# Performance work log

Hardware: AMD Instinct MI355X
Metric: run time of the kernel (lower is better)

## Reference

```python
import jax, jax.numpy as jnp
import numpy as np

NB, NA, NG, T = 16, 3, 64, 60
EPS = 1e-16


def cal_gous(pd, gt):
    # pd: [N,4], gt: [M,4], boxes as (cx, cy, w, h), normalized. Returns IoU, GIoU [N,M].
    px1 = pd[:, 0] - pd[:, 2] / 2; px2 = pd[:, 0] + pd[:, 2] / 2
    py1 = pd[:, 1] - pd[:, 3] / 2; py2 = pd[:, 1] + pd[:, 3] / 2
    gx1 = gt[:, 0] - gt[:, 2] / 2; gx2 = gt[:, 0] + gt[:, 2] / 2
    gy1 = gt[:, 1] - gt[:, 3] / 2; gy2 = gt[:, 1] + gt[:, 3] / 2
    iw = jnp.clip(jnp.minimum(px2[:, None], gx2[None, :]) - jnp.maximum(px1[:, None], gx1[None, :]), 0.0)
    ih = jnp.clip(jnp.minimum(py2[:, None], gy2[None, :]) - jnp.maximum(py1[:, None], gy1[None, :]), 0.0)
    inter = iw * ih
    pa = (pd[:, 2] * pd[:, 3])[:, None]
    ga = (gt[:, 2] * gt[:, 3])[None, :]
    union = pa + ga - inter
    iou = inter / (union + EPS)
    cw = jnp.maximum(px2[:, None], gx2[None, :]) - jnp.minimum(px1[:, None], gx1[None, :])
    ch = jnp.maximum(py2[:, None], gy2[None, :]) - jnp.minimum(py1[:, None], gy1[None, :])
    ca = cw * ch
    gou = iou - (ca - union) / (ca + EPS)
    return iou, gou


def build_target(labels, nB, nA, nG):
    # Vectorized version of my_build_target: occurrence-rank anchor assignment + scatter.
    g = labels[:, 1:] * nG
    gxs, gys, gws, ghs = g[:, 0], g[:, 1], g[:, 2], g[:, 3]
    b = labels[:, 0].astype(jnp.int32)
    gi = gxs.astype(jnp.int32)
    gj = gys.astype(jnp.int32)
    key = (b * nG + gj) * nG + gi  # cell identity incl. batch
    n = labels.shape[0]
    le = jnp.arange(n)[:, None] <= jnp.arange(n)[None, :]
    # occ[j] = number of earlier (or same) targets sharing the cell, minus 1 -> anchor slot
    occ = ((key[:, None] == key[None, :]) & le).sum(axis=0) - 1
    a = jnp.minimum(occ, nA)  # targets with occ >= nA scatter into dummy slot nA (discarded)

    def scat(vals):
        return jnp.zeros((nB, nA + 1, nG, nG), jnp.float32).at[b, a, gj, gi].set(vals)[:, :nA]

    tx = scat(gxs - jnp.floor(gxs))
    ty = scat(gys - jnp.floor(gys))
    tw = scat(gws / nG)
    th = scat(ghs / nG)
    obj = jnp.zeros((nB, nA + 1, nG, nG), bool).at[b, a, gj, gi].set(True)[:, :nA]
    return obj, tx, ty, tw, th


def _forward(out, labels, int_out, heatmaps):
    nb, nc, nG, _ = out.shape
    nA = nc // 5
    N = nA * nG * nG
    Tn = labels.shape[0] // nb  # equal targets per image by construction
    pred = out.reshape(nb, nA, 5, nG, nG).transpose(0, 1, 3, 4, 2)
    s = jax.nn.sigmoid(pred)
    xs, ys, ws, hs, conf = (s[..., i] for i in range(5))
    gx = jnp.arange(nG, dtype=jnp.float32)[None, None, None, :]
    gy = jnp.arange(nG, dtype=jnp.float32)[None, None, :, None]
    pd_bboxes = jnp.stack([(xs + gx) / nG, (ys + gy) / nG, ws, hs], axis=-1)

    obj, tx, ty, tw, th = build_target(labels, nb, nA, nG)
    objf = obj.astype(jnp.float32)
    cnt = objf.sum()
    loss_xy = (((xs - tx) ** 2 + (ys - ty) ** 2) * objf).sum() / cnt
    tw_s = jnp.where(obj, tw, 1.0); th_s = jnp.where(obj, th, 1.0)
    ws_s = jnp.where(obj, ws, 1.0); hs_s = jnp.where(obj, hs, 1.0)
    loss_wh = (((jnp.log(ws_s) - jnp.log(tw_s)) ** 2 + (jnp.log(hs_s) - jnp.log(th_s)) ** 2) * objf).sum() / cnt

    gts_b = labels.reshape(nb, Tn, 5)[:, :, 1:]
    ious, gous = jax.vmap(cal_gous)(pd_bboxes.reshape(nb, N, 4), gts_b)  # [nb,N,T]
    pd_gous = gous.max(axis=2)
    indices = gous.argmax(axis=2)
    pd_ious = jnp.take_along_axis(ious, indices[..., None], axis=2)[..., 0]  # [nb,N]
    mask = pd_ious >= 0.5
    gt_gous = gous.max(axis=1)
    inds = gous.argmax(axis=1)  # [nb,T] best pred per gt
    loss_gou = jnp.mean(1.0 - gt_gous)
    iou_best = jnp.take_along_axis(ious, inds[:, None, :], axis=1)[:, 0, :]
    loss_iou = jnp.mean(1.0 - iou_best)
    mask_ = jax.vmap(lambda i: jnp.zeros((N,), bool).at[i].set(True))(inds)
    mask2 = (mask | mask_).astype(jnp.float32)
    ignore = ((~mask) | mask_).astype(jnp.float32)
    c2 = mask2.sum(axis=1)
    loss_gou = loss_gou + jnp.mean(((1.0 - pd_gous) * mask2).sum(1) / c2)
    loss_iou = loss_iou + jnp.mean(((1.0 - pd_ious) * mask2).sum(1) / c2)

    conf_f = conf.reshape(nb, N)
    tconfb = (obj.reshape(nb, N) | mask_).astype(jnp.float32)
    inter = (conf_f * tconfb * ignore).sum(1)
    pa = (conf_f ** 2 * ignore).sum(1)
    ga = (tconfb * ignore).sum(1)  # tconfb^2 == tconfb
    loss_conf_b = jnp.mean(1.0 - (2.0 * inter + 1.0) / (pa + ga + 1.0))
    ig = (conf * objf).sum(); pg = (conf ** 2).sum(); gg = objf.sum()
    dice_g = (2.0 * ig + 1.0) / (pg + gg + 1.0)
    dice_g = jnp.where(jnp.isnan(dice_g), 1.0, dice_g)
    loss_conf = (1.0 - dice_g) + loss_conf_b

    total = loss_xy + loss_wh + loss_conf + loss_gou
    heatmap_loss = jnp.mean((int_out - heatmaps) ** 2, axis=(1, 2, 3, 4)).sum() / 4.0
    return jnp.stack([loss_xy, loss_wh, loss_conf, loss_iou, loss_gou, total, heatmap_loss])


def setup_inputs() -> dict:
    key = jax.random.key(0)
    k1, k2, k3, k4, k5 = jax.random.split(key, 5)
    out = jax.random.normal(k1, (NB, NA * 5, NG, NG), jnp.float32)
    b = jnp.repeat(jnp.arange(NB), T).astype(jnp.float32)
    xy = jax.random.uniform(k2, (NB * T, 2), jnp.float32, 0.02, 0.98)
    wh = jax.random.uniform(k3, (NB * T, 2), jnp.float32, 0.05, 0.30)
    labels = jnp.concatenate([b[:, None], xy, wh], axis=1)  # [nGts,5]: (batch, cx, cy, w, h)
    int_out = jax.random.uniform(k4, (4, NB, NA, NG, NG), jnp.float32)
    heatmaps = jax.random.uniform(k5, (4, NB, NA, NG, NG), jnp.float32)
    return {"out": out, "labels": labels, "int_out": int_out, "heatmaps": heatmaps}


def reference(out, labels, int_out, heatmaps):
    return _forward(out, labels, int_out, heatmaps)
```

## Files before the change

### kernel.cpp

```cpp
#include <hip/hip_runtime.h>

#define NBATCH 16
#define NANCH  3
#define NGRID  64
#define NT     60
#define NPB    (NANCH*NGRID*NGRID)
#define NCELL  (NBATCH*NPB)
#define NLBL   (NBATCH*NT)
#define NBPB   (NPB/256)
#define NBLKB  (NBATCH*NBPB)
#define FEPS   1e-16f

__device__ __forceinline__ float frcp(float x) { return __builtin_amdgcn_rcpf(x); }
__device__ __forceinline__ float sigm(float x) { return frcp(1.0f + __expf(-x)); }

__device__ __forceinline__ float waveSum(float v) {
#pragma unroll
    for (int o = 32; o > 0; o >>= 1) v += __shfl_down(v, o, 64);
    return v;
}
__device__ __forceinline__ double waveSumD(double v) {
#pragma unroll
    for (int o = 32; o > 0; o >>= 1) v += __shfl_down(v, o, 64);
    return v;
}

__device__ __forceinline__ unsigned int ford(float f) {
    unsigned int u = __float_as_uint(f);
    return (u & 0x80000000u) ? ~u : (u | 0x80000000u);
}
__device__ __forceinline__ float ford_inv(unsigned int u) {
    unsigned int v = (u & 0x80000000u) ? (u & 0x7fffffffu) : ~u;
    return __uint_as_float(v);
}

__device__ __forceinline__ float gou_f(float px1, float py1, float px2, float py2, float pa,
                                       float gx1, float gy1, float gx2, float gy2, float ga) {
    float iw = fmaxf(fminf(px2, gx2) - fmaxf(px1, gx1), 0.f);
    float ih = fmaxf(fminf(py2, gy2) - fmaxf(py1, gy1), 0.f);
    float inter = iw * ih;
    float un = pa + ga - inter;
    float cw = fmaxf(px2, gx2) - fminf(px1, gx1);
    float ch = fmaxf(py2, gy2) - fminf(py1, gy1);
    float ca = cw * ch;
    float ue = un + FEPS, ce = ca + FEPS;
    return (inter * ce - (ca - un) * ue) * frcp(ue * ce);
}
__device__ __forceinline__ float iou_f(float px1, float py1, float px2, float py2, float pa,
                                       float gx1, float gy1, float gx2, float gy2, float ga) {
    float iw = fmaxf(fminf(px2, gx2) - fmaxf(px1, gx1), 0.f);
    float ih = fmaxf(fminf(py2, gy2) - fmaxf(py1, gy1), 0.f);
    float inter = iw * ih;
    float un = pa + ga - inter;
    return inter * frcp(un + FEPS);
}

__global__ __launch_bounds__(256)
void kB(const float* __restrict__ out, const float* __restrict__ labels,
        const float4* __restrict__ io4, const float4* __restrict__ hm4,
        unsigned long long* __restrict__ gtpart, float4* __restrict__ gtaux,
        double* __restrict__ bpart, unsigned int* __restrict__ ticket) {
    int blk = blockIdx.x, thr = threadIdx.x;
    if (blk == 0 && thr == 0) *ticket = 0u;

    int b = blk / NBPB;
    int s = blk - b * NBPB;
    int n = s * 256 + thr;
    int idx = b * NPB + n;
    int wave = thr >> 6, lane = thr & 63;

    __shared__ float4 G4[NT];
    __shared__ float  GA[NT];
    __shared__ float4 Bxy[256];
    __shared__ float  Bpa[256];
    __shared__ float  pdG[256], pdI[256], cfL[256];
    __shared__ unsigned long long W[4][NT];
    __shared__ unsigned int obits[8];
    __shared__ int keys[NT];
    __shared__ float red[8][4];

    if (thr < 8) obits[thr] = 0u;
    if (thr < NT) {
        const float* lp = labels + (b * NT + thr) * 5;
        float gx = lp[1], gy = lp[2], gw = lp[3], gh = lp[4];
        G4[thr] = make_float4(gx - gw * 0.5f, gy - gh * 0.5f,
                              gx + gw * 0.5f, gy + gh * 0.5f);
        GA[thr] = gw * gh;
        keys[thr] = ((int)(gy * (float)NGRID) << 6) | (int)(gx * (float)NGRID);
    }

    int a = n >> 12, gj = (n >> 6) & 63, gi = n & 63;
    int base = ((b * NANCH * 5 + a * 5) * NGRID + gj) * NGRID + gi;
    float xs = sigm(out[base]);
    float ys = sigm(out[base + NGRID * NGRID]);
    float ws = sigm(out[base + 2 * NGRID * NGRID]);
    float hs = sigm(out[base + 3 * NGRID * NGRID]);
    float cf = sigm(out[base + 4 * NGRID * NGRID]);

    float bx = (xs + (float)gi) * (1.0f / NGRID);
    float by = (ys + (float)gj) * (1.0f / NGRID);
    float px1 = bx - ws * 0.5f, px2 = bx + ws * 0.5f;
    float py1 = by - hs * 0.5f, py2 = by + hs * 0.5f;
    float pa = ws * hs;

    Bxy[thr] = make_float4(px1, py1, px2, py2);
    Bpa[thr] = pa;
    cfL[thr] = cf;
    __syncthreads();

    if (thr < NT) {
        int key = keys[thr];
        int occ = 0;
        for (int i = 0; i < thr; ++i)
            if (keys[i] == key) occ++;
        if (occ < NANCH) {
            int cell = (occ << 12) | key;
            int lc = cell - s * 256;
            if (lc >= 0 && lc < 256) atomicOr(&obits[lc >> 5], 1u << (lc & 31));
        }
    }

    float bg = -1e30f;
    int bt = 0;
    for (int t = 0; t < NT; ++t) {
        float4 g = G4[t];
        float gou = gou_f(px1, py1, px2, py2, pa, g.x, g.y, g.z, g.w, GA[t]);
        if (gou > bg) { bg = gou; bt = t; }
    }
    float4 gbt = G4[bt];
    float biou = iou_f(px1, py1, px2, py2, pa, gbt.x, gbt.y, gbt.z, gbt.w, GA[bt]);
    pdG[thr] = bg;
    pdI[thr] = biou;

    {
        int t = (lane < NT) ? lane : 0;
        float4 g = G4[t];
        float ga = GA[t];
        int cbase = wave * 64;
        int nbase = s * 256 + cbase;
        unsigned long long bp = 0ull;
#pragma unroll 4
        for (int i = 0; i < 64; ++i) {
            float4 p = Bxy[cbase + i];
            float cpa = Bpa[cbase + i];
            float gou = gou_f(p.x, p.y, p.z, p.w, cpa, g.x, g.y, g.z, g.w, ga);
            unsigned long long pk = ((unsigned long long)ford(gou) << 32)
                                  | (0xFFFFFFFFu - (unsigned int)(nbase + i));
            if (pk > bp) bp = pk;
        }
        if (lane < NT) W[wave][lane] = bp;
    }
    __syncthreads();

    if (thr < NT) {
        unsigned long long pk = W[0][thr];
        if (W[1][thr] > pk) pk = W[1][thr];
        if (W[2][thr] > pk) pk = W[2][thr];
        if (W[3][thr] > pk) pk = W[3][thr];
        int wn = (int)(0xFFFFFFFFu - (unsigned int)(pk & 0xFFFFFFFFu));
        int lc = wn - s * 256;
        float4 p = Bxy[lc];
        float4 g = G4[thr];
        float iw = iou_f(p.x, p.y, p.z, p.w, Bpa[lc], g.x, g.y, g.z, g.w, GA[thr]);
        gtpart[blk * 64 + thr] = pk;
        gtaux [blk * 64 + thr] = make_float4(iw, cfL[lc], pdG[lc], pdI[lc]);
    }

    bool mk = (biou >= 0.5f);
    bool ob = (obits[thr >> 5] >> (thr & 31)) & 1u;
    float fmk = mk ? 1.f : 0.f, fnmk = 1.f - fmk, fob = ob ? 1.f : 0.f;
    float4 ha = io4[idx], hb = hm4[idx];
    float d0 = ha.x - hb.x, d1 = ha.y - hb.y, d2 = ha.z - hb.z, d3 = ha.w - hb.w;
    float vals[8] = {
        fmk,
        (1.f - bg) * fmk,
        (1.f - biou) * fmk,
        cf * fob * fnmk,
        cf * cf * fnmk,
        fob * fnmk,
        cf * cf,
        d0 * d0 + d1 * d1 + d2 * d2 + d3 * d3
    };
#pragma unroll
    for (int k = 0; k < 8; ++k) {
        float vv = waveSum(vals[k]);
        if (lane == 0) red[k][wave] = vv;
    }
    __syncthreads();
    if (thr == 0) {
#pragma unroll
        for (int k = 0; k < 8; ++k)
            bpart[blk * 8 + k] = (double)(red[k][0] + red[k][1] + red[k][2] + red[k][3]);
    }
}

__global__ __launch_bounds__(256)
void kD(const float* __restrict__ out, const float* __restrict__ labels,
        const unsigned long long* __restrict__ gtpart, const float4* __restrict__ gtaux,
        const double* __restrict__ bpart,
        double* __restrict__ bacc, unsigned int* __restrict__ ticket,
        float* __restrict__ outp) {
    int b = blockIdx.x, thr = threadIdx.x;
    int wave = thr >> 6, lane = thr & 63;

    __shared__ int keys[NT];
    __shared__ unsigned int obits[NPB / 32];
    __shared__ int wnL[NT];
    __shared__ float4 auxL[NT];
    __shared__ int finS;
    __shared__ double baccL[256];

    for (int w = thr; w < NPB / 32; w += 256) obits[w] = 0u;
    if (thr < NT) {
        const float* lp = labels + (b * NT + thr) * 5;
        keys[thr] = ((int)(lp[2] * (float)NGRID) << 6) | (int)(lp[1] * (float)NGRID);
    }
    __syncthreads();

    float sxy = 0.f, swh = 0.f, sig_ = 0.f, scnt = 0.f, sgou = 0.f, siou = 0.f;
    if (thr < NT) {
        int key = keys[thr];
        int occ = 0;
        for (int i = 0; i < thr; ++i)
            if (keys[i] == key) occ++;
        const float* lp = labels + (b * NT + thr) * 5;
        float bxf = lp[1] * (float)NGRID;
        float byf = lp[2] * (float)NGRID;
        float lw_ = lp[3], lh_ = lp[4];
        int gi = (int)bxf, gj = (int)byf;
        if (occ < NANCH) {
            int cell = (occ << 12) | (gj << 6) | gi;
            atomicOr(&obits[cell >> 5], 1u << (cell & 31));
            int base = ((b * NANCH * 5 + occ * 5) * NGRID + gj) * NGRID + gi;
            float xs = sigm(out[base]);
            float ys = sigm(out[base + NGRID * NGRID]);
            float ws = sigm(out[base + 2 * NGRID * NGRID]);
            float hs = sigm(out[base + 3 * NGRID * NGRID]);
            float cfl = sigm(out[base + 4 * NGRID * NGRID]);
            float tx = bxf - floorf(bxf);
            float ty = byf - floorf(byf);
            float dx = xs - tx, dy = ys - ty;
            sxy = dx * dx + dy * dy;
            float dw = __logf(ws) - __logf(lw_);
            float dh = __logf(hs) - __logf(lh_);
            swh = dw * dw + dh * dh;
            sig_ = cfl;
            scnt = 1.f;
        }
        unsigned long long bestp = 0ull;
        int sbest = 0;
        for (int ss = 0; ss < NBPB; ++ss) {
            unsigned long long pk = gtpart[(b * NBPB + ss) * 64 + thr];
            if (pk > bestp) { bestp = pk; sbest = ss; }
        }
        float4 aux = gtaux[(b * NBPB + sbest) * 64 + thr];
        wnL[thr] = (int)(0xFFFFFFFFu - (unsigned int)(bestp & 0xFFFFFFFFu));
        auxL[thr] = aux;
        sgou = 1.f - ford_inv((unsigned int)(bestp >> 32));
        siou = 1.f - aux.x;
    }
    __syncthreads();

    float dc2 = 0.f, dsg = 0.f, dsi = 0.f, dsint = 0.f, dspa = 0.f, dsga = 0.f;
    if (thr < NT) {
        int wn = wnL[thr];
        bool uniq = true;
        for (int tp = 0; tp < thr; ++tp)
            if (wnL[tp] == wn) { uniq = false; break; }
        if (uniq) {
            float4 aux = auxL[thr];
            bool mk = (aux.w >= 0.5f);
            bool ob = (obits[wn >> 5] >> (wn & 31)) & 1u;
            float fnmk = mk ? 0.f : 1.f;
            float obnmk = (ob ? 1.f : 0.f) * fnmk;
            dc2 = fnmk;
            dsg = (1.f - aux.z) * fnmk;
            dsi = (1.f - aux.w) * fnmk;
            dsint = aux.y * (1.f - obnmk);
            dspa = aux.y * aux.y * (mk ? 1.f : 0.f);
            dsga = 1.f - obnmk;
        }
    }

    double labD[6], corD[6], prtD[8];
    if (wave == 0) {
        labD[0] = (double)waveSum(sxy);
        labD[1] = (double)waveSum(swh);
        labD[2] = (double)waveSum(sig_);
        labD[3] = (double)waveSum(scnt);
        labD[4] = (double)waveSum(sgou);
        labD[5] = (double)waveSum(siou);
        corD[0] = (double)waveSum(dc2);
        corD[1] = (double)waveSum(dsg);
        corD[2] = (double)waveSum(dsi);
        corD[3] = (double)waveSum(dsint);
        corD[4] = (double)waveSum(dspa);
        corD[5] = (double)waveSum(dsga);
#pragma unroll
        for (int k = 0; k < 8; ++k) {
            double v = (lane < NBPB) ? bpart[(b * NBPB + lane) * 8 + k] : 0.0;
            prtD[k] = waveSumD(v);
        }
    }
    __syncthreads();

    if (thr == 0) {
        double* row = &bacc[b * 16];
        row[0]  = prtD[0] + corD[0];
        row[1]  = prtD[1] + corD[1];
        row[2]  = prtD[2] + corD[2];
        row[3]  = prtD[3] + corD[3];
        row[4]  = prtD[4] + corD[4];
        row[5]  = prtD[5] + corD[5];
        row[6]  = labD[4];
        row[7]  = labD[5];
        row[8]  = labD[0];
        row[9]  = labD[1];
        row[10] = labD[2];
        row[11] = labD[3];
        row[12] = prtD[6];
        row[13] = prtD[7];
        row[14] = 0.0; row[15] = 0.0;
        __threadfence();
        unsigned int old = atomicAdd(ticket, 1u);
        finS = (old == NBATCH - 1) ? 1 : 0;
    }
    __syncthreads();

    if (finS) {
        int bb = thr >> 4, k = thr & 15;
        baccL[thr] = atomicAdd(&bacc[bb * 16 + k], 0.0);
        __syncthreads();
        if (thr == 0) {
            double cnt = 0, sxyT = 0, swhT = 0, igT = 0, pgT = 0, hmT = 0;
            double sgouT = 0, siouT = 0, gou2 = 0, iou2 = 0, confbT = 0;
            for (int q = 0; q < NBATCH; ++q) {
                const double* r = &baccL[q * 16];
                cnt += r[11]; sxyT += r[8]; swhT += r[9]; igT += r[10];
                pgT += r[12]; hmT += r[13];
                sgouT += r[6]; siouT += r[7];
                gou2 += r[1] / r[0];
                iou2 += r[2] / r[0];
                confbT += 1.0 - (2.0 * r[3] + 1.0) / (r[4] + r[5] + 1.0);
            }
            double lxy = sxyT / cnt;
            double lwh = swhT / cnt;
            double lgou = sgouT / (double)NLBL + gou2 / (double)NBATCH;
            double liou = siouT / (double)NLBL + iou2 / (double)NBATCH;
            double dice = (2.0 * igT + 1.0) / (pgT + cnt + 1.0);
            if (dice != dice) dice = 1.0;
            double lconf = 1.0 - dice + confbT / (double)NBATCH;
            double total = lxy + lwh + lconf + lgou;
            double hmv = hmT / (double)(4 * NCELL);
            outp[0] = (float)lxy;
            outp[1] = (float)lwh;
            outp[2] = (float)lconf;
            outp[3] = (float)liou;
            outp[4] = (float)lgou;
            outp[5] = (float)total;
            outp[6] = (float)hmv;
        }
    }
}

extern "C" void kernel_launch(void* const* d_in, const int* in_sizes, int n_in,
                              void* d_out, int out_size, void* d_ws, size_t ws_size,
                              hipStream_t stream) {
    const float* out_p  = (const float*)d_in[0];
    const float* labels = (const float*)d_in[1];
    const float4* io4   = (const float4*)d_in[2];
    const float4* hm4   = (const float4*)d_in[3];
    float* o = (float*)d_out;

    char* ws = (char*)d_ws;
    unsigned long long* gtpart = (unsigned long long*)(ws);
    float4* gtaux = (float4*)(ws + 393216);
    double* bpart = (double*)(ws + 1179648);
    double* bacc  = (double*)(ws + 1228800);
    unsigned int* ticket = (unsigned int*)(ws + 1230848);

    hipLaunchKernelGGL(kB, dim3(NBLKB), dim3(256), 0, stream, out_p, labels, io4, hm4,
                       gtpart, gtaux, bpart, ticket);
    hipLaunchKernelGGL(kD, dim3(NBATCH), dim3(256), 0, stream, out_p, labels,
                       gtpart, gtaux, bpart, bacc, ticket, o);
}
```

Measured before the change: 48.86 us.

## Share the GIoU matrix via LDS instead of recomputing per prediction

```diff
diff --git a/kernel.cpp b/kernel.cpp
--- a/kernel.cpp
+++ b/kernel.cpp
@@ -73,6 +73,7 @@
     __shared__ float  GA[NT];
     __shared__ float4 Bxy[256];
     __shared__ float  Bpa[256];
+    __shared__ float  GM[128][61];
     __shared__ float  pdG[256], pdI[256], cfL[256];
     __shared__ unsigned long long W[4][NT];
     __shared__ unsigned int obits[8];
@@ -120,36 +121,52 @@
         }
     }
 
-    float bg = -1e30f;
-    int bt = 0;
-    for (int t = 0; t < NT; ++t) {
-        float4 g = G4[t];
-        float gou = gou_f(px1, py1, px2, py2, pa, g.x, g.y, g.z, g.w, GA[t]);
-        if (gou > bg) { bg = gou; bt = t; }
-    }
-    float4 gbt = G4[bt];
-    float biou = iou_f(px1, py1, px2, py2, pa, gbt.x, gbt.y, gbt.z, gbt.w, GA[bt]);
-    pdG[thr] = bg;
-    pdI[thr] = biou;
-
-    {
-        int t = (lane < NT) ? lane : 0;
-        float4 g = G4[t];
-        float ga = GA[t];
-        int cbase = wave * 64;
-        int nbase = s * 256 + cbase;
-        unsigned long long bp = 0ull;
+    int t = (lane < NT) ? lane : 0;
+    float4 gt4 = G4[t];
+    float gta = GA[t];
+    unsigned long long bp = 0ull;
+    float bg = -1e30f, biou = 0.0f;
+
+#pragma unroll
+    for (int h = 0; h < 2; ++h) {
+        int cb = h * 128 + wave * 32;
+        int nb = s * 256 + cb;
 #pragma unroll 4
-        for (int i = 0; i < 64; ++i) {
-            float4 p = Bxy[cbase + i];
-            float cpa = Bpa[cbase + i];
-            float gou = gou_f(p.x, p.y, p.z, p.w, cpa, g.x, g.y, g.z, g.w, ga);
+        for (int i = 0; i < 32; ++i) {
+            int c = cb + i;
+            float4 p = Bxy[c];
+            float cpa = Bpa[c];
+            float gou = gou_f(p.x, p.y, p.z, p.w, cpa,
+                              gt4.x, gt4.y, gt4.z, gt4.w, gta);
+            if (lane < NT) GM[c - h * 128][lane] = gou;
             unsigned long long pk = ((unsigned long long)ford(gou) << 32)
-                                  | (0xFFFFFFFFu - (unsigned int)(nbase + i));
+                                  | (0xFFFFFFFFu - (unsigned int)(nb + i));
             if (pk > bp) bp = pk;
         }
-        if (lane < NT) W[wave][lane] = bp;
-    }
+        __syncthreads();
+
+        if ((thr >> 7) == h) {
+            int lc = thr & 127;
+            float bg0 = -1e30f, bg1 = -1e30f;
+            int bt0 = 0, bt1 = NT / 2;
+#pragma unroll 2
+            for (int tt = 0; tt < NT / 2; ++tt) {
+                float g0 = GM[lc][tt];
+                if (g0 > bg0) { bg0 = g0; bt0 = tt; }
+                float g1 = GM[lc][tt + NT / 2];
+                if (g1 > bg1) { bg1 = g1; bt1 = tt + NT / 2; }
+            }
+            bg = bg0;
+            int bt = bt0;
+            if (bg1 > bg0) { bg = bg1; bt = bt1; }
+            float4 gb = G4[bt];
+            biou = iou_f(px1, py1, px2, py2, pa, gb.x, gb.y, gb.z, gb.w, GA[bt]);
+            pdG[thr] = bg;
+            pdI[thr] = biou;
+        }
+        __syncthreads();
+    }
+    if (lane < NT) W[wave][lane] = bp;
     __syncthreads();
 
     if (thr < NT) {
```

Result: faster. 39.96 us (median of 2 runs) (-18.2%).
